# Kernel tuning notes

Measured on AMD Instinct MI355X. Metric: run time of the kernel, lower is better.

Reference implementation:

```python
import jax, jax.numpy as jnp
import numpy as np

B, S, D, H = 2, 2048, 1024, 16
DK = D // H

def setup_inputs() -> dict:
    key = jax.random.key(0)
    ks = jax.random.split(key, 12)
    def lin(k, shape, fan_in):
        bound = 1.0 / np.sqrt(fan_in)
        return jax.random.uniform(k, shape, jnp.float32, -bound, bound)
    inp = {
        'Q': jax.random.normal(ks[0], (B, S, D), jnp.float32),
        'K': jax.random.normal(ks[1], (B, S, D), jnp.float32),
        'V': jax.random.normal(ks[2], (B, S, D), jnp.float32),
        # padding mask: last 128 key positions of batch element 0 are padding
        'padding_mask': jnp.ones((B, 1, 1, S), jnp.int32).at[0, :, :, -128:].set(0),
        # causal look-ahead mask
        'look_ahead_mask': jnp.tril(jnp.ones((S, S), jnp.int32))[None, None],
        'Wq': lin(ks[3], (D, D), D), 'bq': lin(ks[4], (D,), D),
        'Wk': lin(ks[5], (D, D), D), 'bk': lin(ks[6], (D,), D),
        'Wv': lin(ks[7], (D, D), D), 'bv': lin(ks[8], (D,), D),
        'Wo': lin(ks[9], (D, D), D), 'bo': lin(ks[10], (D,), D),
    }
    return inp

def _split_heads(x):
    # [B,S,D] -> [B,H,S,DK]
    b, s, _ = x.shape
    return x.reshape(b, s, H, DK).transpose(0, 2, 1, 3)

def reference(Q, K, V, padding_mask, look_ahead_mask, Wq, bq, Wk, bk, Wv, bv, Wo, bo):
    q = _split_heads(Q @ Wq.T + bq)  # [B,H,S,DK]
    k = _split_heads(K @ Wk.T + bk)
    v = _split_heads(V @ Wv.T + bv)
    scores = jnp.einsum('bhqd,bhkd->bhqk', q, k) / np.sqrt(DK).astype(np.float32)
    neg_inf = jnp.float32(-jnp.inf)
    scores = jnp.where(padding_mask == 0, neg_inf, scores)
    scores = jnp.where(look_ahead_mask == 0, neg_inf, scores)
    weights = jax.nn.softmax(scores, axis=-1)  # dropout is identity in eval mode
    x = jnp.einsum('bhqk,bhkd->bhqd', weights, v)  # [B,H,S,DK]
    x = x.transpose(0, 2, 1, 3).reshape(Q.shape[0], Q.shape[1], D)
    return x @ Wo.T + bo
```

## Files before the change

### kernel.cpp

```cpp
#include <hip/hip_runtime.h>
#include <hip/hip_bf16.h>

#define B_   2
#define S_   2048
#define D_   1024
#define H_   16
#define DK_  64

typedef unsigned short u16;
typedef __attribute__((ext_vector_type(8))) short bf16x8;
typedef __attribute__((ext_vector_type(4))) float f32x4;

static __device__ __forceinline__ u16 f2bf(float f) {
  union { float f; unsigned u; } v; v.f = f;
  unsigned r = v.u + 0x7FFF + ((v.u >> 16) & 1);
  return (u16)(r >> 16);
}

static __device__ __forceinline__ void gl_lds16(const void* g, void* l) {
  __builtin_amdgcn_global_load_lds(
      (const __attribute__((address_space(1))) void*)g,
      (__attribute__((address_space(3))) void*)l, 16, 0, 0);
}

__global__ void cvt3(const float4* __restrict__ a, const float4* __restrict__ b, const float4* __restrict__ c,
                     ushort4* __restrict__ oa, ushort4* __restrict__ ob, ushort4* __restrict__ oc, int n4) {
  int y = blockIdx.y;
  const float4* in = (y == 0) ? a : (y == 1) ? b : c;
  ushort4* out = (y == 0) ? oa : (y == 1) ? ob : oc;
  int i = blockIdx.x * blockDim.x + threadIdx.x;
  if (i < n4) {
    float4 v = in[i];
    ushort4 r;
    r.x = f2bf(v.x); r.y = f2bf(v.y); r.z = f2bf(v.z); r.w = f2bf(v.w);
    out[i] = r;
  }
}
__global__ void cvt4(const float4* __restrict__ a, const float4* __restrict__ b, const float4* __restrict__ c,
                     const float4* __restrict__ d, ushort4* __restrict__ oa, ushort4* __restrict__ ob,
                     ushort4* __restrict__ oc, ushort4* __restrict__ od, int n4) {
  int y = blockIdx.y;
  const float4* in = (y == 0) ? a : (y == 1) ? b : (y == 2) ? c : d;
  ushort4* out = (y == 0) ? oa : (y == 1) ? ob : (y == 2) ? oc : od;
  int i = blockIdx.x * blockDim.x + threadIdx.x;
  if (i < n4) {
    float4 v = in[i];
    ushort4 r;
    r.x = f2bf(v.x); r.y = f2bf(v.y); r.z = f2bf(v.z); r.w = f2bf(v.w);
    out[i] = r;
  }
}

__launch_bounds__(256, 2)
__global__ void gemm_qkv(const u16* __restrict__ Xq, const u16* __restrict__ Xk, const u16* __restrict__ Xv,
                         const u16* __restrict__ Wq, const u16* __restrict__ Wk, const u16* __restrict__ Wv,
                         const float* __restrict__ bq, const float* __restrict__ bk, const float* __restrict__ bv,
                         u16* __restrict__ outq, u16* __restrict__ outk, u16* __restrict__ outv) {
  const int z = blockIdx.z;
  const u16* Am; const u16* Bm; int m0, n0;
  if (z == 2) { Am = Wv; Bm = Xv; m0 = blockIdx.x * 128; n0 = blockIdx.y * 128; }
  else if (z == 1) { Am = Xk; Bm = Wk; m0 = blockIdx.y * 128; n0 = blockIdx.x * 128; }
  else { Am = Xq; Bm = Wq; m0 = blockIdx.y * 128; n0 = blockIdx.x * 128; }
  const float* bias = (z == 0) ? bq : (z == 1) ? bk : bv;

  __shared__ __align__(16) u16 As[128 * 32];
  __shared__ __align__(16) u16 Bs[128 * 32];

  const int tid = threadIdx.x, lane = tid & 63, w = tid >> 6;
  const int q = lane >> 4, cl = lane & 15;
  const int wr = w >> 1, wc = w & 1;

  f32x4 acc[4][4] = {};

  for (int k0 = 0; k0 < D_; k0 += 32) {
#pragma unroll
    for (int i = 0; i < 2; ++i) {
      int cb = (i * 4 + w) * 64;
      int ch = cb + lane;
      int row = ch >> 2, ko = (ch & 3) << 3;
      gl_lds16(Am + (size_t)(m0 + row) * D_ + k0 + ko, As + cb * 8);
      gl_lds16(Bm + (size_t)(n0 + row) * D_ + k0 + ko, Bs + cb * 8);
    }
    __syncthreads();

    bf16x8 af[4], bfr[4];
#pragma unroll
    for (int r = 0; r < 4; ++r) af[r]  = *(const bf16x8*)(As + (wr * 64 + r * 16 + cl) * 32 + q * 8);
#pragma unroll
    for (int c = 0; c < 4; ++c) bfr[c] = *(const bf16x8*)(Bs + (wc * 64 + c * 16 + cl) * 32 + q * 8);
#pragma unroll
    for (int r = 0; r < 4; ++r)
#pragma unroll
      for (int c = 0; c < 4; ++c)
        acc[r][c] = __builtin_amdgcn_mfma_f32_16x16x32_bf16(af[r], bfr[c], acc[r][c], 0, 0, 0);
    __syncthreads();
  }

  if (z == 2) {
#pragma unroll
    for (int r = 0; r < 4; ++r) {
#pragma unroll
      for (int rr = 0; rr < 4; ++rr) {
        int j = m0 + wr * 64 + r * 16 + q * 4 + rr;
        float bval = bias[j];
        int hh = j >> 6, dk = j & 63;
#pragma unroll
        for (int c = 0; c < 4; ++c) {
          int n = n0 + wc * 64 + c * 16 + cl;
          int bb = n >> 11, s = n & (S_ - 1);
          outv[((size_t)(bb * H_ + hh) * DK_ + dk) * S_ + s] = f2bf(acc[r][c][rr] + bval);
        }
      }
    }
  } else {
    const float scale = (z == 0) ? 0.125f : 1.0f;
    u16* o = (z == 0) ? outq : outk;
#pragma unroll
    for (int c = 0; c < 4; ++c) {
      int j = n0 + wc * 64 + c * 16 + cl;
      float bval = bias[j];
      int hh = j >> 6, dk = j & 63;
#pragma unroll
      for (int r = 0; r < 4; ++r) {
#pragma unroll
        for (int rr = 0; rr < 4; ++rr) {
          int n = m0 + wr * 64 + r * 16 + q * 4 + rr;
          int bb = n >> 11, s = n & (S_ - 1);
          o[((size_t)(bb * H_ + hh) * S_ + s) * DK_ + dk] = f2bf((acc[r][c][rr] + bval) * scale);
        }
      }
    }
  }
}

__launch_bounds__(256, 2)
__global__ void attn(const u16* __restrict__ qh, const u16* __restrict__ kh,
                     const u16* __restrict__ vt, const int* __restrict__ pad,
                     u16* __restrict__ attn_out) {
  __shared__ __align__(16) u16 Ks[64 * 64];
  __shared__ __align__(16) u16 Vs[64 * 64];
  __shared__ __align__(16) u16 Ps[4][16 * 72];
  __shared__ float Kbias[64];

  const int tid = threadIdx.x, lane = tid & 63, w = tid >> 6;
  const int q = lane >> 4, cl = lane & 15;
  const int qt = (int)gridDim.x - 1 - (int)blockIdx.x;
  const int qb = qt * 64, h = blockIdx.y, b = blockIdx.z;

  const u16* Q = qh + (size_t)(b * H_ + h) * S_ * DK_;
  const u16* K = kh + (size_t)(b * H_ + h) * S_ * DK_;
  const u16* V = vt + (size_t)(b * H_ + h) * DK_ * S_;
  const int* pm = pad + b * S_;

  const int qr0 = qb + w * 16;
  bf16x8 qf0 = *(const bf16x8*)(Q + (qr0 + cl) * DK_ + q * 8);
  bf16x8 qf1 = *(const bf16x8*)(Q + (qr0 + cl) * DK_ + 32 + q * 8);

  f32x4 o[4] = {};
  float ls[4] = {0.f, 0.f, 0.f, 0.f};
  u16* Pw = Ps[w];

  const int nkv = qt + 1;
  for (int it = 0; it < nkv; ++it) {
    const int kb = it << 6;
#pragma unroll
    for (int i = 0; i < 2; ++i) {
      int s = (i * 4 + w) * 64 + lane;
      int row = s >> 3;
      int c = (s & 7) ^ (row & 7);
      gl_lds16(K + (size_t)(kb + row) * DK_ + (c << 3), Ks + (size_t)s * 8);
      gl_lds16(V + (size_t)row * S_ + kb + (c << 3), Vs + (size_t)s * 8);
    }
    if (tid < 64) {
      Kbias[tid] = (pm[kb + tid] != 0) ? -6.0f : -3e38f;
    }
    __syncthreads();

    f32x4 sa[4];
#pragma unroll
    for (int ct = 0; ct < 4; ++ct) {
      int rk = ct * 16 + cl;
      int c0 = q ^ (rk & 7);
      bf16x8 kf0 = *(const bf16x8*)(Ks + rk * 64 + (c0 << 3));
      bf16x8 kf1 = *(const bf16x8*)(Ks + rk * 64 + ((c0 ^ 4) << 3));
      f32x4 zz = {};
      zz = __builtin_amdgcn_mfma_f32_16x16x32_bf16(qf0, kf0, zz, 0, 0, 0);
      zz = __builtin_amdgcn_mfma_f32_16x16x32_bf16(qf1, kf1, zz, 0, 0, 0);
      sa[ct] = zz;
    }

    if (it < qt) {
#pragma unroll
      for (int ct = 0; ct < 4; ++ct) {
        float kbv = Kbias[ct * 16 + cl];
#pragma unroll
        for (int rr = 0; rr < 4; ++rr) {
          float p = __expf(sa[ct][rr] + kbv);
          ls[rr] += p;
          Pw[(q * 4 + rr) * 72 + ct * 16 + cl] = f2bf(p);
        }
      }
    } else {
#pragma unroll
      for (int ct = 0; ct < 4; ++ct) {
        int kg = kb + ct * 16 + cl;
        float kbv = Kbias[ct * 16 + cl];
#pragma unroll
        for (int rr = 0; rr < 4; ++rr) {
          int qg = qr0 + q * 4 + rr;
          float p = (kg <= qg) ? __expf(sa[ct][rr] + kbv) : 0.f;
          ls[rr] += p;
          Pw[(q * 4 + rr) * 72 + ct * 16 + cl] = f2bf(p);
        }
      }
    }

    bf16x8 pf0 = *(const bf16x8*)(Pw + cl * 72 + q * 8);
    bf16x8 pf1 = *(const bf16x8*)(Pw + cl * 72 + 32 + q * 8);

#pragma unroll
    for (int ct = 0; ct < 4; ++ct) {
      int rv = ct * 16 + cl;
      int c0 = q ^ (rv & 7);
      bf16x8 vf0 = *(const bf16x8*)(Vs + rv * 64 + (c0 << 3));
      bf16x8 vf1 = *(const bf16x8*)(Vs + rv * 64 + ((c0 ^ 4) << 3));
      o[ct] = __builtin_amdgcn_mfma_f32_16x16x32_bf16(pf0, vf0, o[ct], 0, 0, 0);
      o[ct] = __builtin_amdgcn_mfma_f32_16x16x32_bf16(pf1, vf1, o[ct], 0, 0, 0);
    }
    __syncthreads();
  }

#pragma unroll
  for (int rr = 0; rr < 4; ++rr) {
    float l = ls[rr];
    l += __shfl_xor(l, 1, 64);
    l += __shfl_xor(l, 2, 64);
    l += __shfl_xor(l, 4, 64);
    l += __shfl_xor(l, 8, 64);
    float inv = 1.0f / l;
    int qg = qr0 + q * 4 + rr;
    size_t base = (size_t)(b * S_ + qg) * D_ + h * DK_;
#pragma unroll
    for (int ct = 0; ct < 4; ++ct)
      attn_out[base + ct * 16 + cl] = f2bf(o[ct][rr] * inv);
  }
}

__launch_bounds__(256, 2)
__global__ void gemm_out(const u16* __restrict__ A, const u16* __restrict__ W,
                         const float* __restrict__ bias, float* __restrict__ out) {
  __shared__ __align__(16) u16 As[128 * 32];
  __shared__ __align__(16) u16 Bs[128 * 32];

  const int tid = threadIdx.x, lane = tid & 63, w = tid >> 6;
  const int q = lane >> 4, cl = lane & 15;
  const int wr = w >> 1, wc = w & 1;
  const int m0 = blockIdx.y * 128, n0 = blockIdx.x * 128;

  f32x4 acc[4][4] = {};

  for (int k0 = 0; k0 < D_; k0 += 32) {
#pragma unroll
    for (int i = 0; i < 2; ++i) {
      int cb = (i * 4 + w) * 64;
      int ch = cb + lane;
      int row = ch >> 2, ko = (ch & 3) << 3;
      gl_lds16(A + (size_t)(m0 + row) * D_ + k0 + ko, As + cb * 8);
      gl_lds16(W + (size_t)(n0 + row) * D_ + k0 + ko, Bs + cb * 8);
    }
    __syncthreads();

    bf16x8 af[4], bfr[4];
#pragma unroll
    for (int r = 0; r < 4; ++r) af[r]  = *(const bf16x8*)(As + (wr * 64 + r * 16 + cl) * 32 + q * 8);
#pragma unroll
    for (int c = 0; c < 4; ++c) bfr[c] = *(const bf16x8*)(Bs + (wc * 64 + c * 16 + cl) * 32 + q * 8);
#pragma unroll
    for (int r = 0; r < 4; ++r)
#pragma unroll
      for (int c = 0; c < 4; ++c)
        acc[r][c] = __builtin_amdgcn_mfma_f32_16x16x32_bf16(af[r], bfr[c], acc[r][c], 0, 0, 0);
    __syncthreads();
  }

#pragma unroll
  for (int c = 0; c < 4; ++c) {
    int j = n0 + wc * 64 + c * 16 + cl;
    float bval = bias[j];
#pragma unroll
    for (int r = 0; r < 4; ++r) {
#pragma unroll
      for (int rr = 0; rr < 4; ++rr) {
        int n = m0 + wr * 64 + r * 16 + q * 4 + rr;
        out[(size_t)n * D_ + j] = acc[r][c][rr] + bval;
      }
    }
  }
}

extern "C" void kernel_launch(void* const* d_in, const int* in_sizes, int n_in,
                              void* d_out, int out_size, void* d_ws, size_t ws_size,
                              hipStream_t stream) {
  const float* Qf  = (const float*)d_in[0];
  const float* Kf  = (const float*)d_in[1];
  const float* Vf  = (const float*)d_in[2];
  const int*   pad = (const int*)d_in[3];
  const float* Wqf = (const float*)d_in[5];
  const float* bq  = (const float*)d_in[6];
  const float* Wkf = (const float*)d_in[7];
  const float* bk  = (const float*)d_in[8];
  const float* Wvf = (const float*)d_in[9];
  const float* bv  = (const float*)d_in[10];
  const float* Wof = (const float*)d_in[11];
  const float* bo  = (const float*)d_in[12];

  const size_t BSD = (size_t)B_ * S_ * D_;
  const size_t DD  = (size_t)D_ * D_;

  char* ws = (char*)d_ws;
  u16* Qb   = (u16*)ws; ws += BSD * 2;
  u16* Kb   = (u16*)ws; ws += BSD * 2;
  u16* Vb   = (u16*)ws; ws += BSD * 2;
  u16* Wqb  = (u16*)ws; ws += DD * 2;
  u16* Wkb  = (u16*)ws; ws += DD * 2;
  u16* Wvb  = (u16*)ws; ws += DD * 2;
  u16* Wob  = (u16*)ws; ws += DD * 2;
  u16* qhd  = (u16*)ws; ws += BSD * 2;
  u16* khd  = (u16*)ws; ws += BSD * 2;
  u16* vtd  = (u16*)ws; ws += BSD * 2;
  u16* attn_o = (u16*)ws; ws += BSD * 2;

  const int n4 = (int)(BSD / 4);
  const int w4 = (int)(DD / 4);
  dim3 gc3(n4 / 256, 3), gc4(w4 / 256, 4);
  cvt3<<<gc3, 256, 0, stream>>>((const float4*)Qf, (const float4*)Kf, (const float4*)Vf,
                                (ushort4*)Qb, (ushort4*)Kb, (ushort4*)Vb, n4);
  cvt4<<<gc4, 256, 0, stream>>>((const float4*)Wqf, (const float4*)Wkf, (const float4*)Wvf, (const float4*)Wof,
                                (ushort4*)Wqb, (ushort4*)Wkb, (ushort4*)Wvb, (ushort4*)Wob, w4);

  dim3 g1(D_ / 128, (B_ * S_) / 128, 3);
  gemm_qkv<<<g1, 256, 0, stream>>>(Qb, Kb, Vb, Wqb, Wkb, Wvb, bq, bk, bv, qhd, khd, vtd);

  dim3 g2(S_ / 64, H_, B_);
  attn<<<g2, 256, 0, stream>>>(qhd, khd, vtd, pad, attn_o);

  dim3 g3(D_ / 128, (B_ * S_) / 128);
  gemm_out<<<g3, 256, 0, stream>>>(attn_o, Wob, bo, (float*)d_out);
}
```

Measured before the change: 257.2 us.

## Shrink GEMM tiles to 128x64, fuse conversion kernels, use exp2 softmax

```diff
diff --git a/kernel.cpp b/kernel.cpp
--- a/kernel.cpp
+++ b/kernel.cpp
@@ -11,6 +11,9 @@
 typedef __attribute__((ext_vector_type(8))) short bf16x8;
 typedef __attribute__((ext_vector_type(4))) float f32x4;
 
+#define QSCALE   0.18033688011112042f
+#define SMBIAS  -8.656170245333781f
+
 static __device__ __forceinline__ u16 f2bf(float f) {
   union { float f; unsigned u; } v; v.f = f;
   unsigned r = v.u + 0x7FFF + ((v.u >> 16) & 1);
@@ -23,73 +26,76 @@
       (__attribute__((address_space(3))) void*)l, 16, 0, 0);
 }
 
-__global__ void cvt3(const float4* __restrict__ a, const float4* __restrict__ b, const float4* __restrict__ c,
-                     ushort4* __restrict__ oa, ushort4* __restrict__ ob, ushort4* __restrict__ oc, int n4) {
+__global__ void cvt_all(const float4* __restrict__ s0, const float4* __restrict__ s1,
+                        const float4* __restrict__ s2, const float4* __restrict__ s3,
+                        const float4* __restrict__ s4, const float4* __restrict__ s5,
+                        const float4* __restrict__ s6,
+                        ushort4* __restrict__ d0, ushort4* __restrict__ d1,
+                        ushort4* __restrict__ d2, ushort4* __restrict__ d3,
+                        ushort4* __restrict__ d4, ushort4* __restrict__ d5,
+                        ushort4* __restrict__ d6, int nbig, int nsmall) {
   int y = blockIdx.y;
-  const float4* in = (y == 0) ? a : (y == 1) ? b : c;
-  ushort4* out = (y == 0) ? oa : (y == 1) ? ob : oc;
+  const float4* in; ushort4* out; int n;
+  switch (y) {
+    case 0: in = s0; out = d0; n = nbig; break;
+    case 1: in = s1; out = d1; n = nbig; break;
+    case 2: in = s2; out = d2; n = nbig; break;
+    case 3: in = s3; out = d3; n = nsmall; break;
+    case 4: in = s4; out = d4; n = nsmall; break;
+    case 5: in = s5; out = d5; n = nsmall; break;
+    default: in = s6; out = d6; n = nsmall; break;
+  }
   int i = blockIdx.x * blockDim.x + threadIdx.x;
-  if (i < n4) {
+  if (i < n) {
     float4 v = in[i];
     ushort4 r;
     r.x = f2bf(v.x); r.y = f2bf(v.y); r.z = f2bf(v.z); r.w = f2bf(v.w);
     out[i] = r;
   }
 }
-__global__ void cvt4(const float4* __restrict__ a, const float4* __restrict__ b, const float4* __restrict__ c,
-                     const float4* __restrict__ d, ushort4* __restrict__ oa, ushort4* __restrict__ ob,
-                     ushort4* __restrict__ oc, ushort4* __restrict__ od, int n4) {
-  int y = blockIdx.y;
-  const float4* in = (y == 0) ? a : (y == 1) ? b : (y == 2) ? c : d;
-  ushort4* out = (y == 0) ? oa : (y == 1) ? ob : (y == 2) ? oc : od;
-  int i = blockIdx.x * blockDim.x + threadIdx.x;
-  if (i < n4) {
-    float4 v = in[i];
-    ushort4 r;
-    r.x = f2bf(v.x); r.y = f2bf(v.y); r.z = f2bf(v.z); r.w = f2bf(v.w);
-    out[i] = r;
-  }
-}
-
-__launch_bounds__(256, 2)
+
+__launch_bounds__(256, 4)
 __global__ void gemm_qkv(const u16* __restrict__ Xq, const u16* __restrict__ Xk, const u16* __restrict__ Xv,
                          const u16* __restrict__ Wq, const u16* __restrict__ Wk, const u16* __restrict__ Wv,
                          const float* __restrict__ bq, const float* __restrict__ bk, const float* __restrict__ bv,
                          u16* __restrict__ outq, u16* __restrict__ outk, u16* __restrict__ outv) {
   const int z = blockIdx.z;
+  const int bid = blockIdx.x;
   const u16* Am; const u16* Bm; int m0, n0;
-  if (z == 2) { Am = Wv; Bm = Xv; m0 = blockIdx.x * 128; n0 = blockIdx.y * 128; }
-  else if (z == 1) { Am = Xk; Bm = Wk; m0 = blockIdx.y * 128; n0 = blockIdx.x * 128; }
-  else { Am = Xq; Bm = Wq; m0 = blockIdx.y * 128; n0 = blockIdx.x * 128; }
+  if (z == 2)      { Am = Wv; Bm = Xv; m0 = (bid >> 6) * 128; n0 = (bid & 63) * 64; }
+  else if (z == 1) { Am = Xk; Bm = Wk; m0 = (bid >> 4) * 128; n0 = (bid & 15) * 64; }
+  else             { Am = Xq; Bm = Wq; m0 = (bid >> 4) * 128; n0 = (bid & 15) * 64; }
   const float* bias = (z == 0) ? bq : (z == 1) ? bk : bv;
 
   __shared__ __align__(16) u16 As[128 * 32];
-  __shared__ __align__(16) u16 Bs[128 * 32];
+  __shared__ __align__(16) u16 Bs[64 * 32];
 
   const int tid = threadIdx.x, lane = tid & 63, w = tid >> 6;
   const int q = lane >> 4, cl = lane & 15;
-  const int wr = w >> 1, wc = w & 1;
-
-  f32x4 acc[4][4] = {};
+
+  f32x4 acc[2][4] = {};
 
   for (int k0 = 0; k0 < D_; k0 += 32) {
 #pragma unroll
     for (int i = 0; i < 2; ++i) {
-      int cb = (i * 4 + w) * 64;
-      int ch = cb + lane;
-      int row = ch >> 2, ko = (ch & 3) << 3;
-      gl_lds16(Am + (size_t)(m0 + row) * D_ + k0 + ko, As + cb * 8);
-      gl_lds16(Bm + (size_t)(n0 + row) * D_ + k0 + ko, Bs + cb * 8);
-    }
-    __syncthreads();
-
-    bf16x8 af[4], bfr[4];
-#pragma unroll
-    for (int r = 0; r < 4; ++r) af[r]  = *(const bf16x8*)(As + (wr * 64 + r * 16 + cl) * 32 + q * 8);
-#pragma unroll
-    for (int c = 0; c < 4; ++c) bfr[c] = *(const bf16x8*)(Bs + (wc * 64 + c * 16 + cl) * 32 + q * 8);
-#pragma unroll
-    for (int r = 0; r < 4; ++r)
+      int s = (i * 4 + w) * 64 + lane;
+      int row = s >> 2, ko = (s & 3) << 3;
+      gl_lds16(Am + (size_t)(m0 + row) * D_ + k0 + ko, As + (size_t)s * 8);
+    }
+    {
+      int s = tid;
+      int row = s >> 2, ko = (s & 3) << 3;
+      gl_lds16(Bm + (size_t)(n0 + row) * D_ + k0 + ko, Bs + (size_t)s * 8);
+    }
+    __syncthreads();
+
+    bf16x8 af[2], bfr[4];
+#pragma unroll
+    for (int r = 0; r < 2; ++r) af[r]  = *(const bf16x8*)(As + (w * 32 + r * 16 + cl) * 32 + q * 8);
+#pragma unroll
+    for (int c = 0; c < 4; ++c) bfr[c] = *(const bf16x8*)(Bs + (c * 16 + cl) * 32 + q * 8);
+#pragma unroll
+    for (int r = 0; r < 2; ++r)
 #pragma unroll
       for (int c = 0; c < 4; ++c)
         acc[r][c] = __builtin_amdgcn_mfma_f32_16x16x32_bf16(af[r], bfr[c], acc[r][c], 0, 0, 0);
@@ -98,33 +104,33 @@
 
   if (z == 2) {
 #pragma unroll
-    for (int r = 0; r < 4; ++r) {
+    for (int r = 0; r < 2; ++r) {
 #pragma unroll
       for (int rr = 0; rr < 4; ++rr) {
-        int j = m0 + wr * 64 + r * 16 + q * 4 + rr;
+        int j = m0 + w * 32 + r * 16 + q * 4 + rr;
         float bval = bias[j];
         int hh = j >> 6, dk = j & 63;
 #pragma unroll
         for (int c = 0; c < 4; ++c) {
-          int n = n0 + wc * 64 + c * 16 + cl;
+          int n = n0 + c * 16 + cl;
           int bb = n >> 11, s = n & (S_ - 1);
           outv[((size_t)(bb * H_ + hh) * DK_ + dk) * S_ + s] = f2bf(acc[r][c][rr] + bval);
         }
       }
     }
   } else {
-    const float scale = (z == 0) ? 0.125f : 1.0f;
+    const float scale = (z == 0) ? QSCALE : 1.0f;
     u16* o = (z == 0) ? outq : outk;
 #pragma unroll
     for (int c = 0; c < 4; ++c) {
-      int j = n0 + wc * 64 + c * 16 + cl;
+      int j = n0 + c * 16 + cl;
       float bval = bias[j];
       int hh = j >> 6, dk = j & 63;
 #pragma unroll
-      for (int r = 0; r < 4; ++r) {
+      for (int r = 0; r < 2; ++r) {
 #pragma unroll
         for (int rr = 0; rr < 4; ++rr) {
-          int n = m0 + wr * 64 + r * 16 + q * 4 + rr;
+          int n = m0 + w * 32 + r * 16 + q * 4 + rr;
           int bb = n >> 11, s = n & (S_ - 1);
           o[((size_t)(bb * H_ + hh) * S_ + s) * DK_ + dk] = f2bf((acc[r][c][rr] + bval) * scale);
         }
@@ -172,7 +178,7 @@
       gl_lds16(V + (size_t)row * S_ + kb + (c << 3), Vs + (size_t)s * 8);
     }
     if (tid < 64) {
-      Kbias[tid] = (pm[kb + tid] != 0) ? -6.0f : -3e38f;
+      Kbias[tid] = (pm[kb + tid] != 0) ? SMBIAS : -3e38f;
     }
     __syncthreads();
 
@@ -195,7 +201,7 @@
         float kbv = Kbias[ct * 16 + cl];
 #pragma unroll
         for (int rr = 0; rr < 4; ++rr) {
-          float p = __expf(sa[ct][rr] + kbv);
+          float p = exp2f(sa[ct][rr] + kbv);
           ls[rr] += p;
           Pw[(q * 4 + rr) * 72 + ct * 16 + cl] = f2bf(p);
         }
@@ -208,7 +214,7 @@
 #pragma unroll
         for (int rr = 0; rr < 4; ++rr) {
           int qg = qr0 + q * 4 + rr;
-          float p = (kg <= qg) ? __expf(sa[ct][rr] + kbv) : 0.f;
+          float p = (kg <= qg) ? exp2f(sa[ct][rr] + kbv) : 0.f;
           ls[rr] += p;
           Pw[(q * 4 + rr) * 72 + ct * 16 + cl] = f2bf(p);
         }
@@ -246,37 +252,39 @@
   }
 }
 
-__launch_bounds__(256, 2)
+__launch_bounds__(256, 4)
 __global__ void gemm_out(const u16* __restrict__ A, const u16* __restrict__ W,
                          const float* __restrict__ bias, float* __restrict__ out) {
   __shared__ __align__(16) u16 As[128 * 32];
-  __shared__ __align__(16) u16 Bs[128 * 32];
+  __shared__ __align__(16) u16 Bs[64 * 32];
 
   const int tid = threadIdx.x, lane = tid & 63, w = tid >> 6;
   const int q = lane >> 4, cl = lane & 15;
-  const int wr = w >> 1, wc = w & 1;
-  const int m0 = blockIdx.y * 128, n0 = blockIdx.x * 128;
-
-  f32x4 acc[4][4] = {};
+  const int m0 = blockIdx.y * 128, n0 = blockIdx.x * 64;
+
+  f32x4 acc[2][4] = {};
 
   for (int k0 = 0; k0 < D_; k0 += 32) {
 #pragma unroll
     for (int i = 0; i < 2; ++i) {
-      int cb = (i * 4 + w) * 64;
-      int ch = cb + lane;
-      int row = ch >> 2, ko = (ch & 3) << 3;
-      gl_lds16(A + (size_t)(m0 + row) * D_ + k0 + ko, As + cb * 8);
-      gl_lds16(W + (size_t)(n0 + row) * D_ + k0 + ko, Bs + cb * 8);
-    }
-    __syncthreads();
-
-    bf16x8 af[4], bfr[4];
-#pragma unroll
-    for (int r = 0; r < 4; ++r) af[r]  = *(const bf16x8*)(As + (wr * 64 + r * 16 + cl) * 32 + q * 8);
-#pragma unroll
-    for (int c = 0; c < 4; ++c) bfr[c] = *(const bf16x8*)(Bs + (wc * 64 + c * 16 + cl) * 32 + q * 8);
-#pragma unroll
-    for (int r = 0; r < 4; ++r)
+      int s = (i * 4 + w) * 64 + lane;
+      int row = s >> 2, ko = (s & 3) << 3;
+      gl_lds16(A + (size_t)(m0 + row) * D_ + k0 + ko, As + (size_t)s * 8);
+    }
+    {
+      int s = tid;
+      int row = s >> 2, ko = (s & 3) << 3;
+      gl_lds16(W + (size_t)(n0 + row) * D_ + k0 + ko, Bs + (size_t)s * 8);
+    }
+    __syncthreads();
+
+    bf16x8 af[2], bfr[4];
+#pragma unroll
+    for (int r = 0; r < 2; ++r) af[r]  = *(const bf16x8*)(As + (w * 32 + r * 16 + cl) * 32 + q * 8);
+#pragma unroll
+    for (int c = 0; c < 4; ++c) bfr[c] = *(const bf16x8*)(Bs + (c * 16 + cl) * 32 + q * 8);
+#pragma unroll
+    for (int r = 0; r < 2; ++r)
 #pragma unroll
       for (int c = 0; c < 4; ++c)
         acc[r][c] = __builtin_amdgcn_mfma_f32_16x16x32_bf16(af[r], bfr[c], acc[r][c], 0, 0, 0);
@@ -285,13 +293,13 @@
 
 #pragma unroll
   for (int c = 0; c < 4; ++c) {
-    int j = n0 + wc * 64 + c * 16 + cl;
+    int j = n0 + c * 16 + cl;
     float bval = bias[j];
 #pragma unroll
-    for (int r = 0; r < 4; ++r) {
+    for (int r = 0; r < 2; ++r) {
 #pragma unroll
       for (int rr = 0; rr < 4; ++rr) {
-        int n = m0 + wr * 64 + r * 16 + q * 4 + rr;
+        int n = m0 + w * 32 + r * 16 + q * 4 + rr;
         out[(size_t)n * D_ + j] = acc[r][c][rr] + bval;
       }
     }
@@ -332,18 +340,19 @@
 
   const int n4 = (int)(BSD / 4);
   const int w4 = (int)(DD / 4);
-  dim3 gc3(n4 / 256, 3), gc4(w4 / 256, 4);
-  cvt3<<<gc3, 256, 0, stream>>>((const float4*)Qf, (const float4*)Kf, (const float4*)Vf,
-                                (ushort4*)Qb, (ushort4*)Kb, (ushort4*)Vb, n4);
-  cvt4<<<gc4, 256, 0, stream>>>((const float4*)Wqf, (const float4*)Wkf, (const float4*)Wvf, (const float4*)Wof,
-                                (ushort4*)Wqb, (ushort4*)Wkb, (ushort4*)Wvb, (ushort4*)Wob, w4);
-
-  dim3 g1(D_ / 128, (B_ * S_) / 128, 3);
+  dim3 gc(n4 / 256, 7);
+  cvt_all<<<gc, 256, 0, stream>>>((const float4*)Qf, (const float4*)Kf, (const float4*)Vf,
+                                  (const float4*)Wqf, (const float4*)Wkf, (const float4*)Wvf, (const float4*)Wof,
+                                  (ushort4*)Qb, (ushort4*)Kb, (ushort4*)Vb,
+                                  (ushort4*)Wqb, (ushort4*)Wkb, (ushort4*)Wvb, (ushort4*)Wob,
+                                  n4, w4);
+
+  dim3 g1(512, 1, 3);
   gemm_qkv<<<g1, 256, 0, stream>>>(Qb, Kb, Vb, Wqb, Wkb, Wvb, bq, bk, bv, qhd, khd, vtd);
 
   dim3 g2(S_ / 64, H_, B_);
   attn<<<g2, 256, 0, stream>>>(qhd, khd, vtd, pad, attn_o);
 
-  dim3 g3(D_ / 128, (B_ * S_) / 128);
+  dim3 g3(D_ / 64, (B_ * S_) / 128);
   gemm_out<<<g3, 256, 0, stream>>>(attn_o, Wob, bo, (float*)d_out);
 }
```

After: 273.8 us. +6.4%, slower.
